# Optimization experiments

Measured on AMD Instinct MI355X. Metric: run time of the kernel, lower is better.

Reference implementation:

```python
import jax, jax.numpy as jnp
import numpy as np
import math

EPS = 1e-5
NEG_SLOPE = 0.2

def _patches(x, k=3, s=2):
    # x: (N, C, H, W) -> (N, C, k*k, Ho, Wo); VALID padding, stride s
    N, C = x.shape[0], x.shape[1]
    p = jax.lax.conv_general_dilated_patches(x, (k, k), (s, s), 'VALID')
    return p.reshape(N, C, k * k, p.shape[2], p.shape[3])

def _pacconv(x, guide, w, b, k=3):
    # PacConv2d (gaussian kernel, smooth_kernel_type='none', no normalization)
    xp = _patches(x)                              # (N,Cin,K2,Ho,Wo)
    gp = _patches(guide)                          # (N,Cg,K2,Ho,Wo)
    ctr = (k * k) // 2
    d = gp - gp[:, :, ctr:ctr + 1]
    ker = jnp.exp(-0.5 * jnp.sum(d * d, axis=1, keepdims=True))  # (N,1,K2,Ho,Wo)
    out = jnp.einsum('nckhw,ock->nohw', xp * ker,
                     w.reshape(w.shape[0], w.shape[1], k * k))
    return out + b[None, :, None, None]

def _conv(x, w, b):
    out = jax.lax.conv_general_dilated(x, w, (2, 2), 'VALID',
                                       dimension_numbers=('NCHW', 'OIHW', 'NCHW'))
    return out + b[None, :, None, None]

def _avgpool(x):
    s = jax.lax.reduce_window(x, 0.0, jax.lax.add, (1, 1, 3, 3), (1, 1, 2, 2), 'VALID')
    return s / 9.0

def _lrelu(x):
    return jnp.where(x >= 0, x, NEG_SLOPE * x)

def _bn(x, g, b):
    # training-mode BatchNorm2d (batch stats, biased variance)
    m = jnp.mean(x, axis=(0, 2, 3), keepdims=True)
    v = jnp.mean((x - m) ** 2, axis=(0, 2, 3), keepdims=True)
    xn = (x - m) * jax.lax.rsqrt(v + EPS)
    return xn * g[None, :, None, None] + b[None, :, None, None]

def setup_inputs() -> dict:
    key = jax.random.key(0)
    ks = jax.random.split(key, 12)
    N, Cin, H = 128, 1, 120
    x = jax.random.normal(ks[0], (N, Cin, H, H), jnp.float32)
    guide = jax.random.uniform(ks[1], (N, 1, H, H), jnp.float32)
    def wconv(k, co, ci):
        return jax.random.normal(k, (co, ci, 3, 3), jnp.float32) * (1.0 / math.sqrt(ci * 9))
    w1, b1 = wconv(ks[2], 32, Cin), jnp.zeros((32,), jnp.float32)
    w2, b2 = wconv(ks[3], 64, 32), jnp.zeros((64,), jnp.float32)
    w3, b3 = wconv(ks[4], 128, 64), jnp.zeros((128,), jnp.float32)
    w4, b4 = wconv(ks[5], 256, 128), jnp.zeros((256,), jnp.float32)
    g2, be2 = jnp.ones((64,), jnp.float32), jnp.zeros((64,), jnp.float32)
    g3, be3 = jnp.ones((128,), jnp.float32), jnp.zeros((128,), jnp.float32)
    g4, be4 = jnp.ones((256,), jnp.float32), jnp.zeros((256,), jnp.float32)
    wadv = jax.random.normal(ks[6], (1, 9216), jnp.float32)  # EqualLinear raw weight
    badv = jnp.ones((1,), jnp.float32)                        # bias_init=1
    return {"x": x, "guide": guide, "w1": w1, "b1": b1, "w2": w2, "b2": b2,
            "w3": w3, "b3": b3, "w4": w4, "b4": b4, "g2": g2, "be2": be2,
            "g3": g3, "be3": be3, "g4": g4, "be4": be4, "wadv": wadv, "badv": badv}

def reference(x, guide, w1, b1, w2, b2, w3, b3, w4, b4,
              g2, be2, g3, be3, g4, be4, wadv, badv):
    out = _lrelu(_conv(x, w1, b1))                 # (N,32,59,59)
    guide = _avgpool(guide)                        # (N,1,59,59)
    out = _bn(_lrelu(_pacconv(out, guide, w2, b2)), g2, be2)   # (N,64,29,29)
    guide = _avgpool(guide)                        # (N,1,29,29)
    out = _bn(_lrelu(_pacconv(out, guide, w3, b3)), g3, be3)   # (N,128,14,14)
    guide = _avgpool(guide)                        # (N,1,14,14)
    out = _bn(_lrelu(_pacconv(out, guide, w4, b4)), g4, be4)   # (N,256,6,6)
    flat = out.reshape(out.shape[0], -1)           # (N,9216)
    scale = 1.0 / math.sqrt(9216)
    validity = flat @ (wadv * scale).T + badv      # EqualLinear, lr_mul=1
    return validity
```

## Files before the change

### kernel.cpp

```cpp
#include <hip/hip_runtime.h>
#include <hip/hip_bf16.h>

#define EPSBN 1e-5f
#define NEG_SLOPE 0.2f

using f32x4  = __attribute__((ext_vector_type(4))) float;
using bf16x8 = __attribute__((ext_vector_type(8))) short;

#define O_Y1B     0
#define O_G1      7129088
#define O_Y2B     7574656
#define O_G2      11019392
#define O_WKB2    11127040
#define O_WKB3    11136256
#define O_WKB4    11173120
#define O_WADVR   11320576
#define O_ACC     11329792
#define O_G3      11336960
#define O_Y3B     11362048
#define O_Y4B     12967680
#define A_ACC2    0
#define A_ACC3    1024
#define A_ACC4    3072

__device__ __forceinline__ unsigned short f2bf(float f) {
  union { __hip_bfloat16 b; unsigned short u; } cv;
  cv.b = __float2bfloat16(f);
  return cv.u;
}
__device__ __forceinline__ float bf2f(unsigned short u) {
  union { unsigned int i; float f; } x; x.i = (unsigned int)u << 16; return x.f;
}

struct KParams {
  const float *x, *gd, *w1, *b1, *w2, *b2, *w3, *b3, *w4, *b4;
  const float *bg2, *bb2, *bg3, *bb3, *bg4, *bb4, *wadv, *badv;
  float* out;
  float* ws;
};

__global__ __launch_bounds__(256, 2) void k_prep(KParams p) {
  __shared__ float xs[360];
  __shared__ float wsm[320];
  __shared__ unsigned short ysm[1888];
  const int vb = blockIdx.x, tid = threadIdx.x;
  float* ws = p.ws;
  if (vb < 7552) {
    const int n = vb / 59, oh = vb % 59;
    for (int i = tid; i < 320; i += 256)
      wsm[i] = (i < 288) ? p.w1[(i & 31) * 9 + (i >> 5)] : p.b1[i - 288];
    const float* src = p.x + ((size_t)n * 120 + oh * 2) * 120;
    for (int i = tid; i < 360; i += 256) xs[i] = src[i];
    __syncthreads();
    const int co = tid & 31;
    const int ow0 = (tid >> 5) * 8;
    float w[9];
#pragma unroll
    for (int k = 0; k < 9; ++k) w[k] = wsm[k * 32 + co];
    const float bias = wsm[288 + co];
#pragma unroll
    for (int j = 0; j < 8; ++j) {
      int ow = ow0 + j;
      if (ow < 59) {
        float acc = bias;
#pragma unroll
        for (int kh = 0; kh < 3; ++kh)
#pragma unroll
          for (int kw = 0; kw < 3; ++kw)
            acc += xs[kh * 120 + ow * 2 + kw] * w[kh * 3 + kw];
        acc = acc >= 0.0f ? acc : NEG_SLOPE * acc;
        ysm[ow * 32 + co] = f2bf(acc);
      }
    }
    __syncthreads();
    unsigned int* dst = (unsigned int*)((unsigned short*)(ws + O_Y1B) +
                                        (size_t)(n * 59 + oh) * 1888);
    const unsigned int* s2 = (const unsigned int*)ysm;
    for (int i = tid; i < 944; i += 256) dst[i] = s2[i];
  } else if (vb < 9293) {
    int idx = (vb - 7552) * 256 + tid;
    if (idx < 445568) {
      int ow = idx % 59; int t = idx / 59; int oh = t % 59; int n = t / 59;
      const float* gb = p.gd + (n * 120 + oh * 2) * 120 + ow * 2;
      float s = 0.0f;
#pragma unroll
      for (int kh = 0; kh < 3; ++kh)
#pragma unroll
        for (int kw = 0; kw < 3; ++kw) s += gb[kh * 120 + kw];
      ws[O_G1 + idx] = s * (1.0f / 9.0f);
    }
  } else if (vb < 10841) {
    int idx = (vb - 9293) * 256 + tid;
    if (idx < 18432) {
      int kk = idx & 31; int t = idx >> 5; int co = t & 63; int tap = t >> 6;
      ((unsigned short*)(ws + O_WKB2))[idx] = f2bf(p.w2[(co * 32 + kk) * 9 + tap]);
    } else if (idx < 92160) {
      int i = idx - 18432;
      int kk = i & 31; int t = i >> 5; int co = t & 127; int t3 = t >> 7;
      int kc = t3 & 1; int tap = t3 >> 1;
      ((unsigned short*)(ws + O_WKB3))[i] = f2bf(p.w3[(co * 64 + kc * 32 + kk) * 9 + tap]);
    } else if (idx < 387072) {
      int i = idx - 92160;
      int kk = i & 31; int t = i >> 5; int co = t & 255; int t3 = t >> 8;
      int kc = t3 & 3; int tap = t3 >> 2;
      ((unsigned short*)(ws + O_WKB4))[i] = f2bf(p.w4[(co * 128 + kc * 32 + kk) * 9 + tap]);
    } else if (idx < 396288) {
      int i = idx - 387072;
      int c = i & 255; int hw = i >> 8;
      ws[O_WADVR + i] = p.wadv[c * 36 + hw] * (1.0f / 96.0f);
    }
  } else {
    int idx = (vb - 10841) * 256 + tid;
    if (idx * 4 < 7168) {
      float4 z = {0.0f, 0.0f, 0.0f, 0.0f};
      *reinterpret_cast<float4*>(ws + O_ACC + idx * 4) = z;
    }
  }
}

__device__ __forceinline__ void pool_body(const float* __restrict__ pin,
                                          float* __restrict__ pgout,
                                          int PHI, int PHO, int vb, int tid,
                                          int PTOT, int THREADS) {
  int idx = vb * THREADS + tid;
  if (idx < PTOT) {
    int ow = idx % PHO; int t = idx / PHO; int oh = t % PHO; int n = t / PHO;
    const float* gb = pin + (n * PHI + oh * 2) * PHI + ow * 2;
    float s = 0.0f;
#pragma unroll
    for (int kh = 0; kh < 3; ++kh)
#pragma unroll
      for (int kw = 0; kw < 3; ++kw) s += gb[kh * PHI + kw];
    pgout[idx] = s * (1.0f / 9.0f);
  }
}

__device__ __forceinline__ void pac2_body(
    int pxblk, int tid,
    const unsigned short* __restrict__ xb, const float* __restrict__ g,
    const unsigned short* __restrict__ wkb, const float* __restrict__ b,
    unsigned short* __restrict__ yb, float* __restrict__ accout) {
  constexpr int HI = 59, HO = 29, CI = 32, CO = 64, S = 9;
  __shared__ unsigned short Bsh[576 * 40];
  __shared__ unsigned short ytile[4][2048];
  __shared__ float ps[4][128];

  const int lane = tid & 63;
  const int wv   = tid >> 6;
  const int l15  = lane & 15;
  const int g8   = (lane >> 4) * 8;

  for (int j = tid; j < 2304; j += 256) {
    int row = j >> 2, q = j & 3;
    *(uint4*)&Bsh[row * 40 + q * 8] = *(const uint4*)(wkb + row * 32 + q * 8);
  }

  float kk[2][9];
  int   xo[2];
#pragma unroll
  for (int mt = 0; mt < 2; ++mt) {
    int pp = pxblk * 128 + (wv * 2 + mt) * 16 + l15;
    int ow = pp % HO, oh = (pp / HO) % HO, n = pp / (HO * HO);
    const float* gn = g + n * (HI * HI);
    float gc = gn[(oh * 2 + 1) * HI + ow * 2 + 1];
#pragma unroll
    for (int t = 0; t < 9; ++t) {
      float d = gn[(oh * 2 + t / 3) * HI + ow * 2 + (t % 3)] - gc;
      kk[mt][t] = __expf(-0.5f * d * d);
    }
    xo[mt] = ((n * HI + oh * 2) * HI + ow * 2) * CI;
  }

  f32x4 acc[2][4];
#pragma unroll
  for (int nt = 0; nt < 4; ++nt) {
    float bv = b[nt * 16 + l15];
#pragma unroll
    for (int mt = 0; mt < 2; ++mt) acc[mt][nt] = (f32x4){bv, bv, bv, bv};
  }

  auto loadA = [&](int i, bf16x8* dst) {
    const int xoff = ((i / 3) * HI + (i % 3)) * CI + g8;
#pragma unroll
    for (int mt = 0; mt < 2; ++mt)
      dst[mt] = *(const bf16x8*)(xb + xo[mt] + xoff);
  };

  bf16x8 bA[3][2];
  loadA(0, bA[0]); loadA(1, bA[1]);
  __syncthreads();

#pragma unroll
  for (int i = 0; i < S; ++i) {
    if (i + 2 < S) loadA(i + 2, bA[(i + 2) % 3]);
    bf16x8 bf[4];
#pragma unroll
    for (int nt = 0; nt < 4; ++nt)
      bf[nt] = *(const bf16x8*)&Bsh[(i * 64 + nt * 16 + l15) * 40 + g8];
    bf16x8 af[2];
#pragma unroll
    for (int mt = 0; mt < 2; ++mt) {
      float v[8];
#pragma unroll
      for (int j = 0; j < 8; ++j) v[j] = bf2f((unsigned short)bA[i % 3][mt][j]);
      const float kv = kk[mt][i];
#pragma unroll
      for (int j = 0; j < 8; ++j) v[j] *= kv;
#pragma unroll
      for (int j = 0; j < 8; ++j) af[mt][j] = (short)f2bf(v[j]);
    }
#pragma unroll
    for (int mt = 0; mt < 2; ++mt)
#pragma unroll
      for (int nt = 0; nt < 4; ++nt)
        acc[mt][nt] = __builtin_amdgcn_mfma_f32_16x16x32_bf16(af[mt], bf[nt], acc[mt][nt], 0, 0, 0);
  }

#pragma unroll
  for (int nt = 0; nt < 4; ++nt) {
    const int coL = nt * 16 + l15;
    float s = 0.0f, q = 0.0f;
#pragma unroll
    for (int mt = 0; mt < 2; ++mt)
#pragma unroll
      for (int r = 0; r < 4; ++r) {
        float v = acc[mt][nt][r];
        v = v >= 0.0f ? v : NEG_SLOPE * v;
        int row = mt * 16 + ((lane >> 4) << 2) + r;
        ytile[wv][row * 64 + nt * 16 + l15] = f2bf(v);
        s += v; q += v * v;
      }
    s += __shfl_xor(s, 16, 64); q += __shfl_xor(q, 16, 64);
    s += __shfl_xor(s, 32, 64); q += __shfl_xor(q, 32, 64);
    if (l15 == lane) { ps[wv][coL * 2 + 0] = s; ps[wv][coL * 2 + 1] = q; }
  }
  __syncthreads();
  {
    unsigned short* dbase = yb + (size_t)(pxblk * 128 + wv * 32) * CO;
    const uint4* srcT = (const uint4*)ytile[wv];
#pragma unroll
    for (int i = 0; i < 4; ++i) {
      int row = i * 8 + (lane >> 3);
      int u4  = lane & 7;
      *(uint4*)(dbase + (size_t)row * CO + u4 * 8) = srcT[row * 8 + u4];
    }
  }
  if (tid < 64) {
    float s = ps[0][tid * 2] + ps[1][tid * 2] + ps[2][tid * 2] + ps[3][tid * 2];
    float q = ps[0][tid * 2 + 1] + ps[1][tid * 2 + 1] + ps[2][tid * 2 + 1] + ps[3][tid * 2 + 1];
    atomicAdd(&accout[((pxblk & 7) * CO + tid) * 2 + 0], s);
    atomicAdd(&accout[((pxblk & 7) * CO + tid) * 2 + 1], q);
  }
}

template <int CI, int CO, int HI, int HO>
__device__ __forceinline__ void pacg_body(
    int pxblk, int cob, int tid,
    const unsigned short* __restrict__ xb, const float* __restrict__ g,
    const unsigned short* __restrict__ wkb, const float* __restrict__ b,
    const float* __restrict__ gamma, const float* __restrict__ beta,
    const float* __restrict__ accin, float invM,
    unsigned short* __restrict__ yb, float* __restrict__ accout) {
  constexpr int KC  = CI / 32;
  constexpr int S   = 9 * KC;
  constexpr int COB = 128;

  __shared__ unsigned short ytile[2][2048];
  __shared__ float ps[COB * 2];
  __shared__ float bscl[CI], bshl[CI];

  const int lane = tid & 63;
  const int wn   = tid >> 6;
  const int l15  = lane & 15;
  const int g8   = (lane >> 4) * 8;
  const int co0  = cob * COB;

  for (int i = tid; i < CI; i += 128) {
    float s = 0.0f, q = 0.0f;
#pragma unroll
    for (int sl = 0; sl < 8; ++sl) {
      s += accin[(sl * CI + i) * 2 + 0];
      q += accin[(sl * CI + i) * 2 + 1];
    }
    float m = s * invM;
    float var = q * invM - m * m;
    float sc = gamma[i] * rsqrtf(var + EPSBN);
    bscl[i] = sc;
    bshl[i] = beta[i] - m * sc;
  }
  __syncthreads();

  float kk[2][9];
  int   xo[2];
#pragma unroll
  for (int mt = 0; mt < 2; ++mt) {
    int pp = pxblk * 32 + mt * 16 + l15;
    int ow = pp % HO, oh = (pp / HO) % HO, n = pp / (HO * HO);
    const float* gn = g + n * (HI * HI);
    float gc = gn[(oh * 2 + 1) * HI + ow * 2 + 1];
#pragma unroll
    for (int t = 0; t < 9; ++t) {
      float d = gn[(oh * 2 + t / 3) * HI + ow * 2 + (t % 3)] - gc;
      kk[mt][t] = __expf(-0.5f * d * d);
    }
    xo[mt] = ((n * HI + oh * 2) * HI + ow * 2) * CI;
  }

  f32x4 acc[2][4];
#pragma unroll
  for (int nt = 0; nt < 4; ++nt) {
    float bv = b[co0 + wn * 64 + nt * 16 + l15];
#pragma unroll
    for (int mt = 0; mt < 2; ++mt) acc[mt][nt] = (f32x4){bv, bv, bv, bv};
  }

  auto loadStep = [&](int i, bf16x8* dA, bf16x8* dB) {
    const int t  = i / KC;
    const int kc = i % KC;
    const int xoff = ((t / 3) * HI + (t % 3)) * CI + kc * 32 + g8;
#pragma unroll
    for (int mt = 0; mt < 2; ++mt)
      dA[mt] = *(const bf16x8*)(xb + xo[mt] + xoff);
#pragma unroll
    for (int nt = 0; nt < 4; ++nt)
      dB[nt] = *(const bf16x8*)(wkb + ((size_t)i * CO + co0 + wn * 64 + nt * 16 + l15) * 32 + g8);
  };

  bf16x8 bA[3][2], bB[3][4];
  loadStep(0, bA[0], bB[0]);
  loadStep(1, bA[1], bB[1]);

#pragma unroll
  for (int i = 0; i < S; ++i) {
    if (i + 2 < S) loadStep(i + 2, bA[(i + 2) % 3], bB[(i + 2) % 3]);
    const int t  = i / KC;
    const int kc = i % KC;
    bf16x8 af[2];
#pragma unroll
    for (int mt = 0; mt < 2; ++mt) {
      float v[8];
#pragma unroll
      for (int j = 0; j < 8; ++j) v[j] = bf2f((unsigned short)bA[i % 3][mt][j]);
      const int c0 = kc * 32 + g8;
#pragma unroll
      for (int j = 0; j < 8; ++j) v[j] = v[j] * bscl[c0 + j] + bshl[c0 + j];
      const float kv = kk[mt][t];
#pragma unroll
      for (int j = 0; j < 8; ++j) v[j] *= kv;
#pragma unroll
      for (int j = 0; j < 8; ++j) af[mt][j] = (short)f2bf(v[j]);
    }
#pragma unroll
    for (int mt = 0; mt < 2; ++mt)
#pragma unroll
      for (int nt = 0; nt < 4; ++nt)
        acc[mt][nt] = __builtin_amdgcn_mfma_f32_16x16x32_bf16(af[mt], bB[i % 3][nt], acc[mt][nt], 0, 0, 0);
  }

#pragma unroll
  for (int nt = 0; nt < 4; ++nt) {
    const int coL = wn * 64 + nt * 16 + l15;
    float s = 0.0f, q = 0.0f;
#pragma unroll
    for (int mt = 0; mt < 2; ++mt)
#pragma unroll
      for (int r = 0; r < 4; ++r) {
        float v = acc[mt][nt][r];
        v = v >= 0.0f ? v : NEG_SLOPE * v;
        int row = mt * 16 + ((lane >> 4) << 2) + r;
        ytile[wn][row * 64 + nt * 16 + l15] = f2bf(v);
        s += v; q += v * v;
      }
    s += __shfl_xor(s, 16, 64); q += __shfl_xor(q, 16, 64);
    s += __shfl_xor(s, 32, 64); q += __shfl_xor(q, 32, 64);
    if (l15 == lane) { ps[coL * 2 + 0] = s; ps[coL * 2 + 1] = q; }
  }
  __syncthreads();
  {
    unsigned short* dbase = yb + (size_t)(pxblk * 32) * CO + co0 + wn * 64;
    const uint4* srcT = (const uint4*)ytile[wn];
#pragma unroll
    for (int i = 0; i < 4; ++i) {
      int row = i * 8 + (lane >> 3);
      int u4  = lane & 7;
      *(uint4*)(dbase + (size_t)row * CO + u4 * 8) = srcT[row * 8 + u4];
    }
  }
  if (tid < COB) {
    atomicAdd(&accout[((pxblk & 7) * CO + co0 + tid) * 2 + 0], ps[tid * 2]);
    atomicAdd(&accout[((pxblk & 7) * CO + co0 + tid) * 2 + 1], ps[tid * 2 + 1]);
  }
}

__global__ __launch_bounds__(256, 2) void k_s1(KParams p) {
  float* ws = p.ws;
  int vb = blockIdx.x;
  if (vb < 841)
    pac2_body(vb, threadIdx.x,
        (unsigned short*)(ws + O_Y1B), ws + O_G1, (const unsigned short*)(ws + O_WKB2),
        p.b2, (unsigned short*)(ws + O_Y2B), ws + O_ACC + A_ACC2);
  else
    pool_body(ws + O_G1, ws + O_G2, 59, 29, vb - 841, threadIdx.x, 107648, 256);
}
__global__ __launch_bounds__(128, 2) void k_s2(KParams p) {
  float* ws = p.ws;
  int vb = blockIdx.x;
  if (vb < 784)
    pacg_body<64, 128, 29, 14>(vb, 0, threadIdx.x,
        (unsigned short*)(ws + O_Y2B), ws + O_G2, (const unsigned short*)(ws + O_WKB3),
        p.b3, p.bg2, p.bb2, ws + O_ACC + A_ACC2, 1.0f / 107648.0f,
        (unsigned short*)(ws + O_Y3B), ws + O_ACC + A_ACC3);
  else
    pool_body(ws + O_G2, ws + O_G3, 29, 14, vb - 784, threadIdx.x, 25088, 128);
}
__global__ __launch_bounds__(128, 2) void k_s3(KParams p) {
  float* ws = p.ws;
  int pxblk = blockIdx.x >> 1, cob = blockIdx.x & 1;
  pacg_body<128, 256, 14, 6>(pxblk, cob, threadIdx.x,
      (unsigned short*)(ws + O_Y3B), ws + O_G3, (const unsigned short*)(ws + O_WKB4),
      p.b4, p.bg3, p.bb3, ws + O_ACC + A_ACC3, 1.0f / 25088.0f,
      (unsigned short*)(ws + O_Y4B), ws + O_ACC + A_ACC4);
}
__global__ __launch_bounds__(256, 2) void k_s4(KParams p) {
  __shared__ float ss[256];
  float* ws = p.ws;
  int n = blockIdx.x, t = threadIdx.x;
  const unsigned short* y4b = (const unsigned short*)(ws + O_Y4B);
  const float* acc4 = ws + O_ACC + A_ACC4;
  float s0 = 0.0f, q0 = 0.0f;
#pragma unroll
  for (int sl = 0; sl < 8; ++sl) {
    s0 += acc4[(sl * 256 + t) * 2 + 0];
    q0 += acc4[(sl * 256 + t) * 2 + 1];
  }
  float m = s0 * (1.0f / 4608.0f);
  float var = q0 * (1.0f / 4608.0f) - m * m;
  float sc = p.bg4[t] * rsqrtf(var + EPSBN);
  float sh = p.bb4[t] - m * sc;
  const float* wadvr = ws + O_WADVR;
  float s = 0.0f;
  for (int j = t; j < 9216; j += 256)
    s += (bf2f(y4b[n * 9216 + j]) * sc + sh) * wadvr[j];
  ss[t] = s; __syncthreads();
  for (int off = 128; off > 0; off >>= 1) {
    if (t < off) ss[t] += ss[t + off];
    __syncthreads();
  }
  if (t == 0) p.out[n] = ss[0] + p.badv[0];
}

extern "C" void kernel_launch(void* const* d_in, const int* in_sizes, int n_in,
                              void* d_out, int out_size, void* d_ws, size_t ws_size,
                              hipStream_t stream) {
  KParams prm;
  prm.x    = (const float*)d_in[0];
  prm.gd   = (const float*)d_in[1];
  prm.w1   = (const float*)d_in[2];
  prm.b1   = (const float*)d_in[3];
  prm.w2   = (const float*)d_in[4];
  prm.b2   = (const float*)d_in[5];
  prm.w3   = (const float*)d_in[6];
  prm.b3   = (const float*)d_in[7];
  prm.w4   = (const float*)d_in[8];
  prm.b4   = (const float*)d_in[9];
  prm.bg2  = (const float*)d_in[10];
  prm.bb2  = (const float*)d_in[11];
  prm.bg3  = (const float*)d_in[12];
  prm.bb3  = (const float*)d_in[13];
  prm.bg4  = (const float*)d_in[14];
  prm.bb4  = (const float*)d_in[15];
  prm.wadv = (const float*)d_in[16];
  prm.badv = (const float*)d_in[17];
  prm.out  = (float*)d_out;
  prm.ws   = (float*)d_ws;

  k_prep<<<10848, 256, 0, stream>>>(prm);
  k_s1<<<1262, 256, 0, stream>>>(prm);
  k_s2<<<980, 128, 0, stream>>>(prm);
  k_s3<<<288, 128, 0, stream>>>(prm);
  k_s4<<<128, 256, 0, stream>>>(prm);
}
```

Baseline: 103.1 us.

## Flatten conv1 to one output per thread and alias shared memory in pac2

The first conv stage in k_prep no longer stages input rows and weights in shared memory. It now uses one thread per output element, reading input and weights directly from global or cache and launching many more blocks. In pac2, the weight tile and the output/stat tiles now share one aliased LDS buffer, separated by an added barrier, which cuts LDS per block. Launch bounds are raised so more blocks can be resident per CU, at the cost of more global reads in conv1 and possible register pressure in the stage kernels.

```diff
diff --git a/kernel.cpp b/kernel.cpp
--- a/kernel.cpp
+++ b/kernel.cpp
@@ -39,46 +39,28 @@
   float* ws;
 };
 
-__global__ __launch_bounds__(256, 2) void k_prep(KParams p) {
-  __shared__ float xs[360];
-  __shared__ float wsm[320];
-  __shared__ unsigned short ysm[1888];
+__global__ __launch_bounds__(256, 8) void k_prep(KParams p) {
   const int vb = blockIdx.x, tid = threadIdx.x;
   float* ws = p.ws;
-  if (vb < 7552) {
-    const int n = vb / 59, oh = vb % 59;
-    for (int i = tid; i < 320; i += 256)
-      wsm[i] = (i < 288) ? p.w1[(i & 31) * 9 + (i >> 5)] : p.b1[i - 288];
-    const float* src = p.x + ((size_t)n * 120 + oh * 2) * 120;
-    for (int i = tid; i < 360; i += 256) xs[i] = src[i];
-    __syncthreads();
-    const int co = tid & 31;
-    const int ow0 = (tid >> 5) * 8;
-    float w[9];
-#pragma unroll
-    for (int k = 0; k < 9; ++k) w[k] = wsm[k * 32 + co];
-    const float bias = wsm[288 + co];
-#pragma unroll
-    for (int j = 0; j < 8; ++j) {
-      int ow = ow0 + j;
-      if (ow < 59) {
-        float acc = bias;
-#pragma unroll
-        for (int kh = 0; kh < 3; ++kh)
-#pragma unroll
-          for (int kw = 0; kw < 3; ++kw)
-            acc += xs[kh * 120 + ow * 2 + kw] * w[kh * 3 + kw];
-        acc = acc >= 0.0f ? acc : NEG_SLOPE * acc;
-        ysm[ow * 32 + co] = f2bf(acc);
-      }
-    }
-    __syncthreads();
-    unsigned int* dst = (unsigned int*)((unsigned short*)(ws + O_Y1B) +
-                                        (size_t)(n * 59 + oh) * 1888);
-    const unsigned int* s2 = (const unsigned int*)ysm;
-    for (int i = tid; i < 944; i += 256) dst[i] = s2[i];
-  } else if (vb < 9293) {
-    int idx = (vb - 7552) * 256 + tid;
+  if (vb < 55696) {
+    int idx = vb * 256 + tid;
+    int co = idx & 31;
+    int t = idx >> 5;
+    int ow = t % 59;
+    int oh = (t / 59) % 59;
+    int n  = t / 3481;
+    const float* xb = p.x + ((size_t)n * 120 + oh * 2) * 120 + ow * 2;
+    const float* wr = p.w1 + co * 9;
+    float acc = p.b1[co];
+#pragma unroll
+    for (int kh = 0; kh < 3; ++kh)
+#pragma unroll
+      for (int kw = 0; kw < 3; ++kw)
+        acc += xb[kh * 120 + kw] * wr[kh * 3 + kw];
+    acc = acc >= 0.0f ? acc : NEG_SLOPE * acc;
+    ((unsigned short*)(ws + O_Y1B))[idx] = f2bf(acc);
+  } else if (vb < 57437) {
+    int idx = (vb - 55696) * 256 + tid;
     if (idx < 445568) {
       int ow = idx % 59; int t = idx / 59; int oh = t % 59; int n = t / 59;
       const float* gb = p.gd + (n * 120 + oh * 2) * 120 + ow * 2;
@@ -89,8 +71,8 @@
         for (int kw = 0; kw < 3; ++kw) s += gb[kh * 120 + kw];
       ws[O_G1 + idx] = s * (1.0f / 9.0f);
     }
-  } else if (vb < 10841) {
-    int idx = (vb - 9293) * 256 + tid;
+  } else if (vb < 58985) {
+    int idx = (vb - 57437) * 256 + tid;
     if (idx < 18432) {
       int kk = idx & 31; int t = idx >> 5; int co = t & 63; int tap = t >> 6;
       ((unsigned short*)(ws + O_WKB2))[idx] = f2bf(p.w2[(co * 32 + kk) * 9 + tap]);
@@ -110,7 +92,7 @@
       ws[O_WADVR + i] = p.wadv[c * 36 + hw] * (1.0f / 96.0f);
     }
   } else {
-    int idx = (vb - 10841) * 256 + tid;
+    int idx = (vb - 58985) * 256 + tid;
     if (idx * 4 < 7168) {
       float4 z = {0.0f, 0.0f, 0.0f, 0.0f};
       *reinterpret_cast<float4*>(ws + O_ACC + idx * 4) = z;
@@ -141,9 +123,10 @@
     const unsigned short* __restrict__ wkb, const float* __restrict__ b,
     unsigned short* __restrict__ yb, float* __restrict__ accout) {
   constexpr int HI = 59, HO = 29, CI = 32, CO = 64, S = 9;
-  __shared__ unsigned short Bsh[576 * 40];
-  __shared__ unsigned short ytile[4][2048];
-  __shared__ float ps[4][128];
+  __shared__ __align__(16) char sm[46080];
+  unsigned short* Bsh   = (unsigned short*)sm;
+  unsigned short* ytile = (unsigned short*)sm;
+  float*          ps    = (float*)(sm + 16384);
 
   const int lane = tid & 63;
   const int wv   = tid >> 6;
@@ -216,6 +199,8 @@
         acc[mt][nt] = __builtin_amdgcn_mfma_f32_16x16x32_bf16(af[mt], bf[nt], acc[mt][nt], 0, 0, 0);
   }
 
+  __syncthreads();
+
 #pragma unroll
   for (int nt = 0; nt < 4; ++nt) {
     const int coL = nt * 16 + l15;
@@ -227,17 +212,17 @@
         float v = acc[mt][nt][r];
         v = v >= 0.0f ? v : NEG_SLOPE * v;
         int row = mt * 16 + ((lane >> 4) << 2) + r;
-        ytile[wv][row * 64 + nt * 16 + l15] = f2bf(v);
+        ytile[wv * 2048 + row * 64 + nt * 16 + l15] = f2bf(v);
         s += v; q += v * v;
       }
     s += __shfl_xor(s, 16, 64); q += __shfl_xor(q, 16, 64);
     s += __shfl_xor(s, 32, 64); q += __shfl_xor(q, 32, 64);
-    if (l15 == lane) { ps[wv][coL * 2 + 0] = s; ps[wv][coL * 2 + 1] = q; }
+    if (l15 == lane) { ps[wv * 128 + coL * 2 + 0] = s; ps[wv * 128 + coL * 2 + 1] = q; }
   }
   __syncthreads();
   {
     unsigned short* dbase = yb + (size_t)(pxblk * 128 + wv * 32) * CO;
-    const uint4* srcT = (const uint4*)ytile[wv];
+    const uint4* srcT = (const uint4*)(ytile + wv * 2048);
 #pragma unroll
     for (int i = 0; i < 4; ++i) {
       int row = i * 8 + (lane >> 3);
@@ -246,8 +231,8 @@
     }
   }
   if (tid < 64) {
-    float s = ps[0][tid * 2] + ps[1][tid * 2] + ps[2][tid * 2] + ps[3][tid * 2];
-    float q = ps[0][tid * 2 + 1] + ps[1][tid * 2 + 1] + ps[2][tid * 2 + 1] + ps[3][tid * 2 + 1];
+    float s = ps[0 * 128 + tid * 2] + ps[1 * 128 + tid * 2] + ps[2 * 128 + tid * 2] + ps[3 * 128 + tid * 2];
+    float q = ps[0 * 128 + tid * 2 + 1] + ps[1 * 128 + tid * 2 + 1] + ps[2 * 128 + tid * 2 + 1] + ps[3 * 128 + tid * 2 + 1];
     atomicAdd(&accout[((pxblk & 7) * CO + tid) * 2 + 0], s);
     atomicAdd(&accout[((pxblk & 7) * CO + tid) * 2 + 1], q);
   }
@@ -392,7 +377,7 @@
   }
 }
 
-__global__ __launch_bounds__(256, 2) void k_s1(KParams p) {
+__global__ __launch_bounds__(256, 3) void k_s1(KParams p) {
   float* ws = p.ws;
   int vb = blockIdx.x;
   if (vb < 841)
@@ -402,7 +387,7 @@
   else
     pool_body(ws + O_G1, ws + O_G2, 59, 29, vb - 841, threadIdx.x, 107648, 256);
 }
-__global__ __launch_bounds__(128, 2) void k_s2(KParams p) {
+__global__ __launch_bounds__(128, 3) void k_s2(KParams p) {
   float* ws = p.ws;
   int vb = blockIdx.x;
   if (vb < 784)
@@ -413,7 +398,7 @@
   else
     pool_body(ws + O_G2, ws + O_G3, 29, 14, vb - 784, threadIdx.x, 25088, 128);
 }
-__global__ __launch_bounds__(128, 2) void k_s3(KParams p) {
+__global__ __launch_bounds__(128, 3) void k_s3(KParams p) {
   float* ws = p.ws;
   int pxblk = blockIdx.x >> 1, cob = blockIdx.x & 1;
   pacg_body<128, 256, 14, 6>(pxblk, cob, threadIdx.x,
@@ -474,7 +459,7 @@
   prm.out  = (float*)d_out;
   prm.ws   = (float*)d_ws;
 
-  k_prep<<<10848, 256, 0, stream>>>(prm);
+  k_prep<<<58992, 256, 0, stream>>>(prm);
   k_s1<<<1262, 256, 0, stream>>>(prm);
   k_s2<<<980, 128, 0, stream>>>(prm);
   k_s3<<<288, 128, 0, stream>>>(prm);
```

Measured after the change: 142.3 us. +38.1%, slower.

## Precompute all guide pools and PAC gaussian kernels per image in prep kernel

Applied to the files above, without the earlier changes.

The three avgpool stages of the guide are folded into one block per image in the prep kernel, using shared memory. The same blocks also precompute the per-pixel 9-tap gaussian kernel tables for all three PAC layers. The PAC stages now read these precomputed tables instead of recomputing exps from the pooled guide, and the extra pool blocks in s1 and s2 are removed. Conv1 blocks now cover 4 output rows each, cutting block count and reloading of weights. The cost is 128 heavy per-image blocks with serial phases, extra LDS use in k_prep, and larger kernel-table workspace traffic.

```diff
diff --git a/kernel.cpp b/kernel.cpp
--- a/kernel.cpp
+++ b/kernel.cpp
@@ -8,17 +8,17 @@
 using bf16x8 = __attribute__((ext_vector_type(8))) short;
 
 #define O_Y1B     0
-#define O_G1      7129088
-#define O_Y2B     7574656
-#define O_G2      11019392
-#define O_WKB2    11127040
-#define O_WKB3    11136256
-#define O_WKB4    11173120
-#define O_WADVR   11320576
-#define O_ACC     11329792
-#define O_G3      11336960
-#define O_Y3B     11362048
-#define O_Y4B     12967680
+#define O_KER2    7129088
+#define O_Y2B     8097920
+#define O_KER3    11542656
+#define O_WKB2    11768448
+#define O_WKB3    11777664
+#define O_WKB4    11814528
+#define O_WADVR   11961984
+#define O_ACC     11971200
+#define O_KER4    11978368
+#define O_Y3B     12019840
+#define O_Y4B     13625472
 #define A_ACC2    0
 #define A_ACC3    1024
 #define A_ACC4    3072
@@ -40,17 +40,24 @@
 };
 
 __global__ __launch_bounds__(256, 2) void k_prep(KParams p) {
-  __shared__ float xs[360];
+  __shared__ float xs[1080];
   __shared__ float wsm[320];
-  __shared__ unsigned short ysm[1888];
+  __shared__ unsigned short ysm[7552];
+  __shared__ float g1s[3481];
+  __shared__ float g2s[841];
+  __shared__ float g3s[196];
   const int vb = blockIdx.x, tid = threadIdx.x;
   float* ws = p.ws;
-  if (vb < 7552) {
-    const int n = vb / 59, oh = vb % 59;
+
+  if (vb < 1920) {
+    const int n = vb / 15, grp = vb % 15;
+    const int oh0 = grp * 4;
+    const int nrows = (59 - oh0) < 4 ? (59 - oh0) : 4;
+    const float* src = p.x + ((size_t)n * 120 + oh0 * 2) * 120;
+    const int nx = (2 * nrows + 1) * 120;
+    for (int i = tid; i < nx; i += 256) xs[i] = src[i];
     for (int i = tid; i < 320; i += 256)
       wsm[i] = (i < 288) ? p.w1[(i & 31) * 9 + (i >> 5)] : p.b1[i - 288];
-    const float* src = p.x + ((size_t)n * 120 + oh * 2) * 120;
-    for (int i = tid; i < 360; i += 256) xs[i] = src[i];
     __syncthreads();
     const int co = tid & 31;
     const int ow0 = (tid >> 5) * 8;
@@ -59,38 +66,96 @@
     for (int k = 0; k < 9; ++k) w[k] = wsm[k * 32 + co];
     const float bias = wsm[288 + co];
 #pragma unroll
-    for (int j = 0; j < 8; ++j) {
-      int ow = ow0 + j;
-      if (ow < 59) {
-        float acc = bias;
-#pragma unroll
-        for (int kh = 0; kh < 3; ++kh)
-#pragma unroll
-          for (int kw = 0; kw < 3; ++kw)
-            acc += xs[kh * 120 + ow * 2 + kw] * w[kh * 3 + kw];
-        acc = acc >= 0.0f ? acc : NEG_SLOPE * acc;
-        ysm[ow * 32 + co] = f2bf(acc);
+    for (int r = 0; r < 4; ++r) {
+      if (r < nrows) {
+#pragma unroll
+        for (int j = 0; j < 8; ++j) {
+          int ow = ow0 + j;
+          if (ow < 59) {
+            float acc = bias;
+#pragma unroll
+            for (int kh = 0; kh < 3; ++kh)
+#pragma unroll
+              for (int kw = 0; kw < 3; ++kw)
+                acc += xs[(2 * r + kh) * 120 + ow * 2 + kw] * w[kh * 3 + kw];
+            acc = acc >= 0.0f ? acc : NEG_SLOPE * acc;
+            ysm[r * 1888 + ow * 32 + co] = f2bf(acc);
+          }
+        }
       }
     }
     __syncthreads();
     unsigned int* dst = (unsigned int*)((unsigned short*)(ws + O_Y1B) +
-                                        (size_t)(n * 59 + oh) * 1888);
+                                       (size_t)(n * 59 + oh0) * 1888);
     const unsigned int* s2 = (const unsigned int*)ysm;
-    for (int i = tid; i < 944; i += 256) dst[i] = s2[i];
-  } else if (vb < 9293) {
-    int idx = (vb - 7552) * 256 + tid;
-    if (idx < 445568) {
-      int ow = idx % 59; int t = idx / 59; int oh = t % 59; int n = t / 59;
-      const float* gb = p.gd + (n * 120 + oh * 2) * 120 + ow * 2;
+    const int nu = nrows * 944;
+    for (int i = tid; i < nu; i += 256) dst[i] = s2[i];
+  } else if (vb < 2048) {
+    const int n = vb - 1920;
+    const float* gdn = p.gd + (size_t)n * 14400;
+    for (int i = tid; i < 3481; i += 256) {
+      int r = i / 59, c = i % 59;
+      const float* gb = gdn + (r * 2) * 120 + c * 2;
       float s = 0.0f;
 #pragma unroll
-      for (int kh = 0; kh < 3; ++kh)
-#pragma unroll
-        for (int kw = 0; kw < 3; ++kw) s += gb[kh * 120 + kw];
-      ws[O_G1 + idx] = s * (1.0f / 9.0f);
-    }
-  } else if (vb < 10841) {
-    int idx = (vb - 9293) * 256 + tid;
+      for (int u = 0; u < 3; ++u)
+#pragma unroll
+        for (int v = 0; v < 3; ++v) s += gb[u * 120 + v];
+      g1s[i] = s * (1.0f / 9.0f);
+    }
+    __syncthreads();
+    for (int i = tid; i < 841; i += 256) {
+      int r = i / 29, c = i % 29;
+      float s = 0.0f;
+#pragma unroll
+      for (int u = 0; u < 3; ++u)
+#pragma unroll
+        for (int v = 0; v < 3; ++v) s += g1s[(r * 2 + u) * 59 + c * 2 + v];
+      g2s[i] = s * (1.0f / 9.0f);
+    }
+    for (int i = tid; i < 841; i += 256) {
+      int oh = i / 29, ow = i % 29;
+      float gc = g1s[(oh * 2 + 1) * 59 + ow * 2 + 1];
+      float* kt = ws + O_KER2 + ((size_t)n * 841 + i) * 9;
+#pragma unroll
+      for (int t = 0; t < 9; ++t) {
+        float d = g1s[(oh * 2 + t / 3) * 59 + ow * 2 + (t % 3)] - gc;
+        kt[t] = __expf(-0.5f * d * d);
+      }
+    }
+    __syncthreads();
+    for (int i = tid; i < 196; i += 256) {
+      int r = i / 14, c = i % 14;
+      float s = 0.0f;
+#pragma unroll
+      for (int u = 0; u < 3; ++u)
+#pragma unroll
+        for (int v = 0; v < 3; ++v) s += g2s[(r * 2 + u) * 29 + c * 2 + v];
+      g3s[i] = s * (1.0f / 9.0f);
+    }
+    for (int i = tid; i < 196; i += 256) {
+      int oh = i / 14, ow = i % 14;
+      float gc = g2s[(oh * 2 + 1) * 29 + ow * 2 + 1];
+      float* kt = ws + O_KER3 + ((size_t)n * 196 + i) * 9;
+#pragma unroll
+      for (int t = 0; t < 9; ++t) {
+        float d = g2s[(oh * 2 + t / 3) * 29 + ow * 2 + (t % 3)] - gc;
+        kt[t] = __expf(-0.5f * d * d);
+      }
+    }
+    __syncthreads();
+    for (int i = tid; i < 36; i += 256) {
+      int oh = i / 6, ow = i % 6;
+      float gc = g3s[(oh * 2 + 1) * 14 + ow * 2 + 1];
+      float* kt = ws + O_KER4 + ((size_t)n * 36 + i) * 9;
+#pragma unroll
+      for (int t = 0; t < 9; ++t) {
+        float d = g3s[(oh * 2 + t / 3) * 14 + ow * 2 + (t % 3)] - gc;
+        kt[t] = __expf(-0.5f * d * d);
+      }
+    }
+  } else if (vb < 3596) {
+    int idx = (vb - 2048) * 256 + tid;
     if (idx < 18432) {
       int kk = idx & 31; int t = idx >> 5; int co = t & 63; int tap = t >> 6;
       ((unsigned short*)(ws + O_WKB2))[idx] = f2bf(p.w2[(co * 32 + kk) * 9 + tap]);
@@ -110,7 +175,7 @@
       ws[O_WADVR + i] = p.wadv[c * 36 + hw] * (1.0f / 96.0f);
     }
   } else {
-    int idx = (vb - 10841) * 256 + tid;
+    int idx = (vb - 3596) * 256 + tid;
     if (idx * 4 < 7168) {
       float4 z = {0.0f, 0.0f, 0.0f, 0.0f};
       *reinterpret_cast<float4*>(ws + O_ACC + idx * 4) = z;
@@ -118,26 +183,9 @@
   }
 }
 
-__device__ __forceinline__ void pool_body(const float* __restrict__ pin,
-                                          float* __restrict__ pgout,
-                                          int PHI, int PHO, int vb, int tid,
-                                          int PTOT, int THREADS) {
-  int idx = vb * THREADS + tid;
-  if (idx < PTOT) {
-    int ow = idx % PHO; int t = idx / PHO; int oh = t % PHO; int n = t / PHO;
-    const float* gb = pin + (n * PHI + oh * 2) * PHI + ow * 2;
-    float s = 0.0f;
-#pragma unroll
-    for (int kh = 0; kh < 3; ++kh)
-#pragma unroll
-      for (int kw = 0; kw < 3; ++kw) s += gb[kh * PHI + kw];
-    pgout[idx] = s * (1.0f / 9.0f);
-  }
-}
-
 __device__ __forceinline__ void pac2_body(
     int pxblk, int tid,
-    const unsigned short* __restrict__ xb, const float* __restrict__ g,
+    const unsigned short* __restrict__ xb, const float* __restrict__ kert,
     const unsigned short* __restrict__ wkb, const float* __restrict__ b,
     unsigned short* __restrict__ yb, float* __restrict__ accout) {
   constexpr int HI = 59, HO = 29, CI = 32, CO = 64, S = 9;
@@ -161,13 +209,9 @@
   for (int mt = 0; mt < 2; ++mt) {
     int pp = pxblk * 128 + (wv * 2 + mt) * 16 + l15;
     int ow = pp % HO, oh = (pp / HO) % HO, n = pp / (HO * HO);
-    const float* gn = g + n * (HI * HI);
-    float gc = gn[(oh * 2 + 1) * HI + ow * 2 + 1];
-#pragma unroll
-    for (int t = 0; t < 9; ++t) {
-      float d = gn[(oh * 2 + t / 3) * HI + ow * 2 + (t % 3)] - gc;
-      kk[mt][t] = __expf(-0.5f * d * d);
-    }
+    const float* kt = kert + (size_t)pp * 9;
+#pragma unroll
+    for (int t = 0; t < 9; ++t) kk[mt][t] = kt[t];
     xo[mt] = ((n * HI + oh * 2) * HI + ow * 2) * CI;
   }
 
@@ -256,7 +300,7 @@
 template <int CI, int CO, int HI, int HO>
 __device__ __forceinline__ void pacg_body(
     int pxblk, int cob, int tid,
-    const unsigned short* __restrict__ xb, const float* __restrict__ g,
+    const unsigned short* __restrict__ xb, const float* __restrict__ kert,
     const unsigned short* __restrict__ wkb, const float* __restrict__ b,
     const float* __restrict__ gamma, const float* __restrict__ beta,
     const float* __restrict__ accin, float invM,
@@ -296,13 +340,9 @@
   for (int mt = 0; mt < 2; ++mt) {
     int pp = pxblk * 32 + mt * 16 + l15;
     int ow = pp % HO, oh = (pp / HO) % HO, n = pp / (HO * HO);
-    const float* gn = g + n * (HI * HI);
-    float gc = gn[(oh * 2 + 1) * HI + ow * 2 + 1];
-#pragma unroll
-    for (int t = 0; t < 9; ++t) {
-      float d = gn[(oh * 2 + t / 3) * HI + ow * 2 + (t % 3)] - gc;
-      kk[mt][t] = __expf(-0.5f * d * d);
-    }
+    const float* kt = kert + (size_t)pp * 9;
+#pragma unroll
+    for (int t = 0; t < 9; ++t) kk[mt][t] = kt[t];
     xo[mt] = ((n * HI + oh * 2) * HI + ow * 2) * CI;
   }
 
@@ -394,30 +434,22 @@
 
 __global__ __launch_bounds__(256, 2) void k_s1(KParams p) {
   float* ws = p.ws;
-  int vb = blockIdx.x;
-  if (vb < 841)
-    pac2_body(vb, threadIdx.x,
-        (unsigned short*)(ws + O_Y1B), ws + O_G1, (const unsigned short*)(ws + O_WKB2),
-        p.b2, (unsigned short*)(ws + O_Y2B), ws + O_ACC + A_ACC2);
-  else
-    pool_body(ws + O_G1, ws + O_G2, 59, 29, vb - 841, threadIdx.x, 107648, 256);
+  pac2_body(blockIdx.x, threadIdx.x,
+      (unsigned short*)(ws + O_Y1B), ws + O_KER2, (const unsigned short*)(ws + O_WKB2),
+      p.b2, (unsigned short*)(ws + O_Y2B), ws + O_ACC + A_ACC2);
 }
 __global__ __launch_bounds__(128, 2) void k_s2(KParams p) {
   float* ws = p.ws;
-  int vb = blockIdx.x;
-  if (vb < 784)
-    pacg_body<64, 128, 29, 14>(vb, 0, threadIdx.x,
-        (unsigned short*)(ws + O_Y2B), ws + O_G2, (const unsigned short*)(ws + O_WKB3),
-        p.b3, p.bg2, p.bb2, ws + O_ACC + A_ACC2, 1.0f / 107648.0f,
-        (unsigned short*)(ws + O_Y3B), ws + O_ACC + A_ACC3);
-  else
-    pool_body(ws + O_G2, ws + O_G3, 29, 14, vb - 784, threadIdx.x, 25088, 128);
+  pacg_body<64, 128, 29, 14>(blockIdx.x, 0, threadIdx.x,
+      (unsigned short*)(ws + O_Y2B), ws + O_KER3, (const unsigned short*)(ws + O_WKB3),
+      p.b3, p.bg2, p.bb2, ws + O_ACC + A_ACC2, 1.0f / 107648.0f,
+      (unsigned short*)(ws + O_Y3B), ws + O_ACC + A_ACC3);
 }
 __global__ __launch_bounds__(128, 2) void k_s3(KParams p) {
   float* ws = p.ws;
   int pxblk = blockIdx.x >> 1, cob = blockIdx.x & 1;
   pacg_body<128, 256, 14, 6>(pxblk, cob, threadIdx.x,
-      (unsigned short*)(ws + O_Y3B), ws + O_G3, (const unsigned short*)(ws + O_WKB4),
+      (unsigned short*)(ws + O_Y3B), ws + O_KER4, (const unsigned short*)(ws + O_WKB4),
       p.b4, p.bg3, p.bb3, ws + O_ACC + A_ACC3, 1.0f / 25088.0f,
       (unsigned short*)(ws + O_Y4B), ws + O_ACC + A_ACC4);
 }
@@ -474,9 +506,9 @@
   prm.out  = (float*)d_out;
   prm.ws   = (float*)d_ws;
 
-  k_prep<<<10848, 256, 0, stream>>>(prm);
-  k_s1<<<1262, 256, 0, stream>>>(prm);
-  k_s2<<<980, 128, 0, stream>>>(prm);
+  k_prep<<<3603, 256, 0, stream>>>(prm);
+  k_s1<<<841, 256, 0, stream>>>(prm);
+  k_s2<<<784, 128, 0, stream>>>(prm);
   k_s3<<<288, 128, 0, stream>>>(prm);
   k_s4<<<128, 256, 0, stream>>>(prm);
 }
```

Measured after the change: 108.3 us. +5.1%, slower.
